# Optimization experiments

Measured on AMD Instinct MI355X. Metric: run time of the kernel, lower is better.

The kernel has to match this reference:

```python
import jax, jax.numpy as jnp
import numpy as np

NUM_GRAPHS = 2048
NODES_PER_GRAPH = 256
N_NODES = NUM_GRAPHS * NODES_PER_GRAPH
N_EDGES = 2 * N_NODES
F_IN = 768
HID = 128
N_CLS = 2


def setup_inputs() -> dict:
    key = jax.random.key(0)
    ks = jax.random.split(key, 12)
    x = jax.random.normal(ks[0], (N_NODES, F_IN), dtype=jnp.float32)
    edge_index = jax.random.randint(ks[1], (2, N_EDGES), 0, N_NODES, dtype=jnp.int32)
    batch = jnp.repeat(jnp.arange(NUM_GRAPHS, dtype=jnp.int32), NODES_PER_GRAPH)
    s = 1.0 / np.sqrt(F_IN)
    sh = 1.0 / np.sqrt(HID)
    s2h = 1.0 / np.sqrt(2 * HID)
    return {
        "x": x,
        "edge_index": edge_index,
        "batch": batch,
        # SAGEConv: lin_l (aggregated neighbors, with bias) + lin_r (root, no bias)
        "W_l": jax.random.uniform(ks[2], (F_IN, HID), jnp.float32, -s, s),
        "b_l": jax.random.uniform(ks[3], (HID,), jnp.float32, -s, s),
        "W_r": jax.random.uniform(ks[4], (F_IN, HID), jnp.float32, -s, s),
        "W0": jax.random.uniform(ks[5], (F_IN, HID), jnp.float32, -s, s),
        "b0": jax.random.uniform(ks[6], (HID,), jnp.float32, -s, s),
        "W1": jax.random.uniform(ks[7], (2 * HID, HID), jnp.float32, -s2h, s2h),
        "b1": jax.random.uniform(ks[8], (HID,), jnp.float32, -s2h, s2h),
        "W2": jax.random.uniform(ks[9], (HID, N_CLS), jnp.float32, -sh, sh),
        "b2": jax.random.uniform(ks[10], (HID,), jnp.float32, -sh, sh)[:N_CLS],
    }


def reference(x, edge_index, batch, W_l, b_l, W_r, W0, b0, W1, b1, W2, b2):
    n = x.shape[0]
    src, dst = edge_index[0], edge_index[1]
    # SAGEConv with mean aggregation: gather -> segment mean -> transform
    msg_sum = jax.ops.segment_sum(x[src], dst, num_segments=n)      # [N, F]
    cnt = jax.ops.segment_sum(jnp.ones((src.shape[0],), x.dtype), dst, num_segments=n)
    agg = msg_sum / jnp.maximum(cnt, 1.0)[:, None]
    h = jax.nn.relu(agg @ W_l + b_l + x @ W_r)                       # [N, H]
    # global max pool per graph
    pooled = jax.ops.segment_max(h, batch, num_segments=NUM_GRAPHS)  # [G, H]
    # root (news) node = first node of each graph (batch is sorted)
    roots = jnp.searchsorted(batch, jnp.arange(NUM_GRAPHS, dtype=batch.dtype))
    news = jax.nn.relu(x[roots] @ W0 + b0)                           # [G, H]
    z = jax.nn.relu(jnp.concatenate([pooled, news], axis=1) @ W1 + b1)
    return jax.nn.log_softmax(z @ W2 + b2, axis=-1)                  # [G, 2]
```

## Files before the change

### kernel.cpp

```cpp
#include <hip/hip_runtime.h>

#define NGRAPH 2048
#define NPG 256
#define NNODE (NGRAPH*NPG)
#define NEDGE (2*NNODE)
#define FIN 768
#define HID 128
#define SLOTS 64
#define BK 64
#define NKT (FIN/BK)

typedef __bf16 bf16x8 __attribute__((ext_vector_type(8)));
typedef __bf16 bf16x4 __attribute__((ext_vector_type(4)));
typedef float f32x4 __attribute__((ext_vector_type(4)));

__device__ __forceinline__ float bflo(unsigned v) {
    return __uint_as_float((v & 0xffffu) << 16);
}
__device__ __forceinline__ float bfhi(unsigned v) {
    return __uint_as_float(v & 0xffff0000u);
}

__global__ __launch_bounds__(256) void k_prep(
    const float* __restrict__ Wl, const float* __restrict__ Wr,
    const float* __restrict__ W0, __bf16* __restrict__ WbT,
    int* __restrict__ deg)
{
    int idx = blockIdx.x * 256 + threadIdx.x;
    deg[idx] = 0;
    if (idx < 384 * FIN) {
        int n = idx / FIN;
        int k = idx - n * FIN;
        float v;
        if (n < HID)            v = Wl[k * HID + n];
        else if (n < 2 * HID)   v = Wr[k * HID + (n - HID)];
        else                    v = W0[k * HID + (n - 2 * HID)];
        WbT[idx] = (__bf16)v;
    }
}

__global__ __launch_bounds__(512, 1) void k_gemm(
    const float* __restrict__ X, const __bf16* __restrict__ WbT,
    __bf16* __restrict__ Yl, __bf16* __restrict__ Yr,
    const int* __restrict__ ei, int* __restrict__ deg, int* __restrict__ elist)
{
    extern __shared__ __align__(16) char sm[];
    const int t = threadIdx.x;

    {
        int e = blockIdx.x * 512 + t;
        int src = ei[e];
        int dst = ei[NEDGE + e];
        int pos = atomicAdd(deg + dst, 1);
        if (pos < SLOTS) elist[(size_t)pos * NNODE + dst] = src;
    }

    const int lane = t & 63;
    const int w = t >> 6;
    const int wr = w >> 2;
    const int wc = w & 3;
    const size_t node0 = (size_t)blockIdx.x * 256;

    f32x4 acc[8][4];
#pragma unroll
    for (int m = 0; m < 8; ++m)
#pragma unroll
        for (int n = 0; n < 4; ++n)
            acc[m][n] = (f32x4){0.f, 0.f, 0.f, 0.f};

    const int arow = t >> 1;
    const int half = t & 1;
    const float* asrc = X + (node0 + arow) * FIN + half * 32;
    const int aswz = (arow & 7) << 4;
    int awoff[4];
#pragma unroll
    for (int j2 = 0; j2 < 4; ++j2)
        awoff[j2] = arow * 128 + (((half * 4 + j2) * 16) ^ aswz);

#define STAGE_B(kt, buf)                                                     \
    {                                                                        \
        _Pragma("unroll")                                                    \
        for (int r = 0; r < 4; ++r) {                                        \
            int idx = r * 512 + t;                                           \
            int bn = idx >> 3, bj = idx & 7;                                 \
            int koff = (bj ^ (bn & 7)) << 3;                                 \
            const __bf16* gp = WbT + bn * FIN + (kt) * BK + koff;            \
            __builtin_amdgcn_global_load_lds(                                \
                (__attribute__((address_space(1))) void*)gp,                 \
                (__attribute__((address_space(3))) void*)((buf) + 32768 + idx * 16),\
                16, 0, 0);                                                   \
        }                                                                    \
    }

    f32x4 q[8];
    STAGE_B(0, sm);
    {
        const f32x4* s4 = (const f32x4*)asrc;
#pragma unroll
        for (int i = 0; i < 8; ++i) q[i] = s4[i];
#pragma unroll
        for (int j2 = 0; j2 < 4; ++j2) {
            bf16x8 h;
#pragma unroll
            for (int i = 0; i < 4; ++i) {
                h[i]     = (__bf16)q[2 * j2][i];
                h[4 + i] = (__bf16)q[2 * j2 + 1][i];
            }
            *(bf16x8*)(sm + awoff[j2]) = h;
        }
    }
    __syncthreads();

    int cur = 0;
    for (int kt = 0; kt < NKT; ++kt) {
        char* bufC = sm + cur * 65536;
        char* bufN = sm + (cur ^ 1) * 65536;
        const bool more = (kt + 1 < NKT);

        if (more) {
            STAGE_B(kt + 1, bufN);
            __builtin_amdgcn_sched_barrier(0);
            const f32x4* s4 = (const f32x4*)(asrc + (kt + 1) * BK);
#pragma unroll
            for (int i = 0; i < 8; ++i) q[i] = s4[i];
            __builtin_amdgcn_sched_barrier(0);
        }

#pragma unroll
        for (int ks = 0; ks < 2; ++ks) {
            const int kb = ks * 64 + ((lane >> 4) << 4);
            bf16x8 a[8], b[4];
#pragma unroll
            for (int m = 0; m < 8; ++m) {
                int row = wr * 128 + m * 16 + (lane & 15);
                a[m] = *(const bf16x8*)(bufC + row * 128 + (kb ^ ((row & 7) << 4)));
            }
#pragma unroll
            for (int n = 0; n < 4; ++n) {
                int col = wc * 64 + n * 16 + (lane & 15);
                b[n] = *(const bf16x8*)(bufC + 32768 + col * 128 + (kb ^ ((col & 7) << 4)));
            }
#pragma unroll
            for (int m = 0; m < 8; ++m)
#pragma unroll
                for (int n = 0; n < 4; ++n)
                    acc[m][n] = __builtin_amdgcn_mfma_f32_16x16x32_bf16(
                        a[m], b[n], acc[m][n], 0, 0, 0);
        }

        if (more) {
#pragma unroll
            for (int j2 = 0; j2 < 4; ++j2) {
                bf16x8 h;
#pragma unroll
                for (int i = 0; i < 4; ++i) {
                    h[i]     = (__bf16)q[2 * j2][i];
                    h[4 + i] = (__bf16)q[2 * j2 + 1][i];
                }
                *(bf16x8*)(bufN + awoff[j2]) = h;
            }
        }
        __syncthreads();
        cur ^= 1;
    }

#pragma unroll
    for (int m = 0; m < 8; ++m) {
        const int rbase = wr * 128 + m * 16 + ((lane >> 4) << 2);
#pragma unroll
        for (int n = 0; n < 4; ++n) {
            const int col = wc * 64 + n * 16 + (lane & 15);
            __bf16* dst = (col < HID) ? Yl : Yr;
            const int c = col & (HID - 1);
#pragma unroll
            for (int j = 0; j < 4; ++j)
                dst[(node0 + rbase + j) * HID + c] = (__bf16)acc[m][n][j];
        }
    }
#undef STAGE_B
}

__global__ __launch_bounds__(512) void k_news(
    const float* __restrict__ X, const __bf16* __restrict__ W0bT,
    const float* __restrict__ b0, float* __restrict__ news)
{
    __shared__ __align__(16) char sm[12288];
    const int t = threadIdx.x;
    const int lane = t & 63;
    const int w = t >> 6;
    const int wr = w >> 2;
    const int wc = w & 3;
    const int g0 = blockIdx.x * 64;

    f32x4 acc[2][2];
#pragma unroll
    for (int m = 0; m < 2; ++m)
#pragma unroll
        for (int n = 0; n < 2; ++n)
            acc[m][n] = (f32x4){0.f, 0.f, 0.f, 0.f};

    const int arow = t >> 3;
    const int ak = (t & 7) * 4;
    const float* asrc = X + (size_t)(g0 + arow) * (NPG * FIN) + ak;
    const int aoff = arow * 64 + (((ak * 2) ^ (((arow >> 1) & 3) << 4)));

    for (int kt = 0; kt < FIN / 32; ++kt) {
        const int k0 = kt * 32;
        __syncthreads();
        {
            f32x4 p = *(const f32x4*)(asrc + k0);
            bf16x4 h;
#pragma unroll
            for (int i = 0; i < 4; ++i) h[i] = (__bf16)p[i];
            *(bf16x4*)(sm + aoff) = h;
        }
        {
            int bn = t >> 2;
            int bj = t & 3;
            int koff = (bj ^ ((bn >> 1) & 3)) << 3;
            const __bf16* g = W0bT + bn * FIN + k0 + koff;
            __builtin_amdgcn_global_load_lds(
                (__attribute__((address_space(1))) void*)g,
                (__attribute__((address_space(3))) void*)(sm + 4096 + t * 16),
                16, 0, 0);
        }
        __syncthreads();

        const int kb = (lane >> 4) << 4;
        bf16x8 a[2], b[2];
#pragma unroll
        for (int m = 0; m < 2; ++m) {
            int row = wr * 32 + m * 16 + (lane & 15);
            a[m] = *(const bf16x8*)(sm + row * 64 + (kb ^ (((row >> 1) & 3) << 4)));
        }
#pragma unroll
        for (int n = 0; n < 2; ++n) {
            int row = wc * 32 + n * 16 + (lane & 15);
            b[n] = *(const bf16x8*)(sm + 4096 + row * 64 + (kb ^ (((row >> 1) & 3) << 4)));
        }
#pragma unroll
        for (int m = 0; m < 2; ++m)
#pragma unroll
            for (int n = 0; n < 2; ++n)
                acc[m][n] = __builtin_amdgcn_mfma_f32_16x16x32_bf16(
                    a[m], b[n], acc[m][n], 0, 0, 0);
    }

#pragma unroll
    for (int m = 0; m < 2; ++m) {
        const int rbase = wr * 32 + m * 16 + ((lane >> 4) << 2);
#pragma unroll
        for (int n = 0; n < 2; ++n) {
            const int col = wc * 32 + n * 16 + (lane & 15);
            const float bb = b0[col];
#pragma unroll
            for (int j = 0; j < 4; ++j)
                news[(size_t)(g0 + rbase + j) * HID + col] =
                    fmaxf(acc[m][n][j] + bb, 0.f);
        }
    }
}

__global__ __launch_bounds__(512) void k_fused(
    const int* __restrict__ deg, const int* __restrict__ elist,
    const __bf16* __restrict__ Yl, const __bf16* __restrict__ Yr,
    const float* __restrict__ bl, const float* __restrict__ news,
    const float* __restrict__ W1, const float* __restrict__ b1,
    const float* __restrict__ W2, const float* __restrict__ b2,
    float* __restrict__ out)
{
    __shared__ int   sdeg[NPG];
    __shared__ int   sel[4 * NPG];
    __shared__ float red[8 * HID];
    __shared__ float cat[2 * HID];
    __shared__ float zs[HID];

    const int g = blockIdx.x;
    const int t = threadIdx.x;
    const size_t gbase = (size_t)g * NPG;

    if (t < NPG) sdeg[t] = deg[gbase + t];
#pragma unroll
    for (int r = 0; r < 2; ++r) {
        int idx = r * 512 + t;
        sel[idx] = elist[(size_t)(idx >> 8) * NNODE + gbase + (idx & 255)];
    }
    __syncthreads();

    const int l = t & 63;
    const int sub = t >> 6;
    const int half = l >> 5;
    const int lj = l & 31;
    const int d4 = lj * 4;
    const float4 blv = *(const float4*)(bl + d4);
    const uint2* yl2 = (const uint2*)Yl;
    const uint2* yr2 = (const uint2*)Yr;

    float m0 = -3.0e38f, m1 = -3.0e38f, m2 = -3.0e38f, m3 = -3.0e38f;

    for (int k4 = 0; k4 < 8; ++k4) {
        const int nA = sub + 8 * (4 * k4 + half);
        const int nB = sub + 8 * (4 * k4 + 2 + half);
        const int dgA = sdeg[nA], dgB = sdeg[nB];
        int sA[4], sB[4];
#pragma unroll
        for (int j = 0; j < 4; ++j) {
            int cA = sel[j * NPG + nA];
            int cB = sel[j * NPG + nB];
            sA[j] = (j < dgA) ? cA : 0;
            sB[j] = (j < dgB) ? cB : 0;
        }
        uint2 vA[4], vB[4];
#pragma unroll
        for (int j = 0; j < 4; ++j) {
            vA[j] = yl2[(size_t)sA[j] * 32 + lj];
            vB[j] = yl2[(size_t)sB[j] * 32 + lj];
        }
        const uint2 yA = yr2[(gbase + nA) * 32 + lj];
        const uint2 yB = yr2[(gbase + nB) * 32 + lj];

        float s0A = 0.f, s1A = 0.f, s2A = 0.f, s3A = 0.f;
        float s0B = 0.f, s1B = 0.f, s2B = 0.f, s3B = 0.f;
#pragma unroll
        for (int j = 0; j < 4; ++j) {
            const float mA = (j < dgA) ? 1.f : 0.f;
            const float mB = (j < dgB) ? 1.f : 0.f;
            s0A = fmaf(mA, bflo(vA[j].x), s0A);
            s1A = fmaf(mA, bfhi(vA[j].x), s1A);
            s2A = fmaf(mA, bflo(vA[j].y), s2A);
            s3A = fmaf(mA, bfhi(vA[j].y), s3A);
            s0B = fmaf(mB, bflo(vB[j].x), s0B);
            s1B = fmaf(mB, bfhi(vB[j].x), s1B);
            s2B = fmaf(mB, bflo(vB[j].y), s2B);
            s3B = fmaf(mB, bfhi(vB[j].y), s3B);
        }
        int mx = dgA > dgB ? dgA : dgB;
        mx = max(mx, __shfl_xor(mx, 32));
        mx = mx < SLOTS ? mx : SLOTS;
        for (int j = 4; j < mx; ++j) {
            int cA = elist[(size_t)j * NNODE + gbase + nA];
            int cB = elist[(size_t)j * NNODE + gbase + nB];
            int eA = (j < dgA) ? cA : 0;
            int eB = (j < dgB) ? cB : 0;
            uint2 wA = yl2[(size_t)eA * 32 + lj];
            uint2 wB = yl2[(size_t)eB * 32 + lj];
            const float mA = (j < dgA) ? 1.f : 0.f;
            const float mB = (j < dgB) ? 1.f : 0.f;
            s0A = fmaf(mA, bflo(wA.x), s0A);
            s1A = fmaf(mA, bfhi(wA.x), s1A);
            s2A = fmaf(mA, bflo(wA.y), s2A);
            s3A = fmaf(mA, bfhi(wA.y), s3A);
            s0B = fmaf(mB, bflo(wB.x), s0B);
            s1B = fmaf(mB, bfhi(wB.x), s1B);
            s2B = fmaf(mB, bflo(wB.y), s2B);
            s3B = fmaf(mB, bfhi(wB.y), s3B);
        }
        const float invA = 1.f / fmaxf((float)dgA, 1.f);
        const float invB = 1.f / fmaxf((float)dgB, 1.f);
        float h0 = fmaf(s0A, invA, blv.x) + bflo(yA.x);
        float h1 = fmaf(s1A, invA, blv.y) + bfhi(yA.x);
        float h2 = fmaf(s2A, invA, blv.z) + bflo(yA.y);
        float h3 = fmaf(s3A, invA, blv.w) + bfhi(yA.y);
        m0 = fmaxf(m0, fmaxf(h0, 0.f));
        m1 = fmaxf(m1, fmaxf(h1, 0.f));
        m2 = fmaxf(m2, fmaxf(h2, 0.f));
        m3 = fmaxf(m3, fmaxf(h3, 0.f));
        h0 = fmaf(s0B, invB, blv.x) + bflo(yB.x);
        h1 = fmaf(s1B, invB, blv.y) + bfhi(yB.x);
        h2 = fmaf(s2B, invB, blv.z) + bflo(yB.y);
        h3 = fmaf(s3B, invB, blv.w) + bfhi(yB.y);
        m0 = fmaxf(m0, fmaxf(h0, 0.f));
        m1 = fmaxf(m1, fmaxf(h1, 0.f));
        m2 = fmaxf(m2, fmaxf(h2, 0.f));
        m3 = fmaxf(m3, fmaxf(h3, 0.f));
    }
    m0 = fmaxf(m0, __shfl_xor(m0, 32));
    m1 = fmaxf(m1, __shfl_xor(m1, 32));
    m2 = fmaxf(m2, __shfl_xor(m2, 32));
    m3 = fmaxf(m3, __shfl_xor(m3, 32));
    if (half == 0) {
        float4 mv = {m0, m1, m2, m3};
        *(float4*)(red + sub * HID + d4) = mv;
    }
    __syncthreads();

    if (t < HID) {
        float v = red[t];
#pragma unroll
        for (int s = 1; s < 8; ++s) v = fmaxf(v, red[s * HID + t]);
        cat[t] = v;
        cat[HID + t] = news[(size_t)g * HID + t];
    }
    __syncthreads();

    if (t < HID) {
        float a0 = 0.f, a1 = 0.f, a2 = 0.f, a3 = 0.f;
        for (int k = 0; k < 2 * HID; k += 4) {
            a0 = fmaf(cat[k + 0], W1[(k + 0) * HID + t], a0);
            a1 = fmaf(cat[k + 1], W1[(k + 1) * HID + t], a1);
            a2 = fmaf(cat[k + 2], W1[(k + 2) * HID + t], a2);
            a3 = fmaf(cat[k + 3], W1[(k + 3) * HID + t], a3);
        }
        zs[t] = fmaxf((a0 + a1) + (a2 + a3) + b1[t], 0.f);
    }
    __syncthreads();

    if (t < 64) {
        float z0 = zs[t * 2], z1 = zs[t * 2 + 1];
        float p0 = fmaf(z0, W2[t * 4 + 0], z1 * W2[t * 4 + 2]);
        float p1 = fmaf(z0, W2[t * 4 + 1], z1 * W2[t * 4 + 3]);
#pragma unroll
        for (int off = 32; off; off >>= 1) {
            p0 += __shfl_down(p0, off);
            p1 += __shfl_down(p1, off);
        }
        if (t == 0) {
            float l0 = p0 + b2[0], l1 = p1 + b2[1];
            float mx = fmaxf(l0, l1);
            float lse = mx + logf(expf(l0 - mx) + expf(l1 - mx));
            out[(size_t)g * 2 + 0] = l0 - lse;
            out[(size_t)g * 2 + 1] = l1 - lse;
        }
    }
}

extern "C" void kernel_launch(void* const* d_in, const int* in_sizes, int n_in,
                              void* d_out, int out_size, void* d_ws, size_t ws_size,
                              hipStream_t stream)
{
    const float* x   = (const float*)d_in[0];
    const int*   ei  = (const int*)d_in[1];
    const float* W_l = (const float*)d_in[3];
    const float* b_l = (const float*)d_in[4];
    const float* W_r = (const float*)d_in[5];
    const float* W0  = (const float*)d_in[6];
    const float* b0  = (const float*)d_in[7];
    const float* W1  = (const float*)d_in[8];
    const float* b1  = (const float*)d_in[9];
    const float* W2  = (const float*)d_in[10];
    const float* b2  = (const float*)d_in[11];
    float* out = (float*)d_out;

    char* ws = (char*)d_ws;
    size_t off = 0;
    auto alloc = [&](size_t bytes) {
        char* p = ws + off;
        off += (bytes + 511) & ~(size_t)511;
        return p;
    };
    __bf16* WbT   = (__bf16*)alloc((size_t)384 * FIN * 2);
    __bf16* Yl    = (__bf16*)alloc((size_t)NNODE * HID * 2);
    __bf16* Yr    = (__bf16*)alloc((size_t)NNODE * HID * 2);
    int*    deg   = (int*)alloc((size_t)NNODE * 4);
    int*    elist = (int*)alloc((size_t)NNODE * SLOTS * 4);
    float*  news  = (float*)alloc((size_t)NGRAPH * HID * 4);
    if (off > ws_size) return;

    k_prep<<<NNODE / 256, 256, 0, stream>>>(W_l, W_r, W0, WbT, deg);
    k_gemm<<<NNODE / 256, 512, 131072, stream>>>(x, WbT, Yl, Yr, ei, deg, elist);
    k_news<<<NGRAPH / 64, 512, 0, stream>>>(x, WbT + (size_t)256 * FIN, b0, news);
    k_fused<<<NGRAPH, 512, 0, stream>>>(deg, elist, Yl, Yr, b_l, news,
                                        W1, b1, W2, b2, out);
}
```

Measured before the change: 668.8 us.

## Stage fp32 X tiles via direct-to-LDS loads and merge news GEMM into main kernel

The main GEMM now copies fp32 X tiles straight into LDS with global_load_lds, using a swizzled layout. The fp32-to-bf16 conversion moves to after the LDS read, and the weight operand is read directly from global memory into registers instead of being staged in LDS. This is meant to take the conversion and register round-trip off the critical path and let the load overlap the MFMA work. The small news GEMM becomes extra blocks of the same launch, removing one kernel launch. The cost is double the LDS traffic for the A operand, since it is now held as fp32, plus uncached global B reads in every tile step.

```diff
diff --git a/kernel.cpp b/kernel.cpp
--- a/kernel.cpp
+++ b/kernel.cpp
@@ -39,13 +39,149 @@
     }
 }
 
+#define AS1 __attribute__((address_space(1)))
+#define AS3 __attribute__((address_space(3)))
+
+template<bool MORE>
+__device__ __forceinline__ void tileF(
+    const char* rbuf, char* sbuf, int t, int lane, int wr, int wc,
+    const float* X, size_t node0, const __bf16* WbT, int kt,
+    f32x4 (&acc)[8][4])
+{
+    bf16x8 b[2][4];
+#pragma unroll
+    for (int ks = 0; ks < 2; ++ks)
+#pragma unroll
+        for (int n = 0; n < 4; ++n) {
+            int col = wc * 64 + n * 16 + (lane & 15);
+            b[ks][n] = *(const bf16x8*)(WbT + (size_t)col * FIN
+                                        + kt * BK + ks * 32 + ((lane >> 4) << 3));
+        }
+    __builtin_amdgcn_sched_barrier(0);
+    if constexpr (MORE) {
+#pragma unroll
+        for (int r = 0; r < 8; ++r) {
+            int idx = r * 512 + t;
+            int row = idx >> 4, s = idx & 15;
+            int koffb = (s * 16) ^ ((row & 7) << 5);
+            const float* g = X + (node0 + row) * FIN + (kt + 1) * BK + (koffb >> 2);
+            __builtin_amdgcn_global_load_lds(
+                (AS1 void*)g, (AS3 void*)(sbuf + idx * 16), 16, 0, 0);
+        }
+        __builtin_amdgcn_sched_barrier(0);
+    }
+#pragma unroll
+    for (int ks = 0; ks < 2; ++ks) {
+        bf16x8 a[8];
+#pragma unroll
+        for (int m = 0; m < 8; ++m) {
+            int row = wr * 128 + m * 16 + (lane & 15);
+            int off = row * 256 + ((ks * 128 + ((lane >> 4) << 5)) ^ ((row & 7) << 5));
+            f32x4 f0 = *(const f32x4*)(rbuf + off);
+            f32x4 f1 = *(const f32x4*)(rbuf + off + 16);
+#pragma unroll
+            for (int i = 0; i < 4; ++i) {
+                a[m][i]     = (__bf16)f0[i];
+                a[m][4 + i] = (__bf16)f1[i];
+            }
+        }
+#pragma unroll
+        for (int m = 0; m < 8; ++m)
+#pragma unroll
+            for (int n = 0; n < 4; ++n)
+                acc[m][n] = __builtin_amdgcn_mfma_f32_16x16x32_bf16(
+                    a[m], b[ks][n], acc[m][n], 0, 0, 0);
+    }
+    if constexpr (MORE) {
+        asm volatile("s_waitcnt vmcnt(0)" ::: "memory");
+        __builtin_amdgcn_s_barrier();
+    }
+}
+
 __global__ __launch_bounds__(512, 1) void k_gemm(
     const float* __restrict__ X, const __bf16* __restrict__ WbT,
     __bf16* __restrict__ Yl, __bf16* __restrict__ Yr,
-    const int* __restrict__ ei, int* __restrict__ deg, int* __restrict__ elist)
+    const int* __restrict__ ei, int* __restrict__ deg, int* __restrict__ elist,
+    const float* __restrict__ b0, float* __restrict__ news)
 {
     extern __shared__ __align__(16) char sm[];
     const int t = threadIdx.x;
+    const int lane = t & 63;
+    const int w = t >> 6;
+
+    if (blockIdx.x >= NNODE / 256) {
+        const int wr = w >> 2;
+        const int wc = w & 3;
+        const int g0 = (blockIdx.x - NNODE / 256) * 64;
+
+        f32x4 acc[2][2];
+#pragma unroll
+        for (int m = 0; m < 2; ++m)
+#pragma unroll
+            for (int n = 0; n < 2; ++n)
+                acc[m][n] = (f32x4){0.f, 0.f, 0.f, 0.f};
+
+        const int arow = t >> 3;
+        const int ak = (t & 7) * 4;
+        const float* asrc = X + (size_t)(g0 + arow) * (NPG * FIN) + ak;
+        const int aoff = arow * 64 + (((ak * 2) ^ (((arow >> 1) & 3) << 4)));
+        const __bf16* W0bT = WbT + (size_t)256 * FIN;
+
+        for (int kt = 0; kt < FIN / 32; ++kt) {
+            const int k0 = kt * 32;
+            __syncthreads();
+            {
+                f32x4 p = *(const f32x4*)(asrc + k0);
+                bf16x4 h;
+#pragma unroll
+                for (int i = 0; i < 4; ++i) h[i] = (__bf16)p[i];
+                *(bf16x4*)(sm + aoff) = h;
+            }
+            {
+                int bn = t >> 2;
+                int bj = t & 3;
+                int koff = (bj ^ ((bn >> 1) & 3)) << 3;
+                const __bf16* g = W0bT + bn * FIN + k0 + koff;
+                __builtin_amdgcn_global_load_lds(
+                    (AS1 void*)g, (AS3 void*)(sm + 4096 + t * 16), 16, 0, 0);
+            }
+            __syncthreads();
+
+            const int kb = (lane >> 4) << 4;
+            bf16x8 a[2], b[2];
+#pragma unroll
+            for (int m = 0; m < 2; ++m) {
+                int row = wr * 32 + m * 16 + (lane & 15);
+                a[m] = *(const bf16x8*)(sm + row * 64 + (kb ^ (((row >> 1) & 3) << 4)));
+            }
+#pragma unroll
+            for (int n = 0; n < 2; ++n) {
+                int row = wc * 32 + n * 16 + (lane & 15);
+                b[n] = *(const bf16x8*)(sm + 4096 + row * 64 + (kb ^ (((row >> 1) & 3) << 4)));
+            }
+#pragma unroll
+            for (int m = 0; m < 2; ++m)
+#pragma unroll
+                for (int n = 0; n < 2; ++n)
+                    acc[m][n] = __builtin_amdgcn_mfma_f32_16x16x32_bf16(
+                        a[m], b[n], acc[m][n], 0, 0, 0);
+        }
+
+#pragma unroll
+        for (int m = 0; m < 2; ++m) {
+            const int rbase = wr * 32 + m * 16 + ((lane >> 4) << 2);
+#pragma unroll
+            for (int n = 0; n < 2; ++n) {
+                const int col = wc * 32 + n * 16 + (lane & 15);
+                const float bb = b0[col];
+#pragma unroll
+                for (int j = 0; j < 4; ++j)
+                    news[(size_t)(g0 + rbase + j) * HID + col] =
+                        fmaxf(acc[m][n][j] + bb, 0.f);
+            }
+        }
+        return;
+    }
 
     {
         int e = blockIdx.x * 512 + t;
@@ -55,8 +191,6 @@
         if (pos < SLOTS) elist[(size_t)pos * NNODE + dst] = src;
     }
 
-    const int lane = t & 63;
-    const int w = t >> 6;
     const int wr = w >> 2;
     const int wc = w & 3;
     const size_t node0 = (size_t)blockIdx.x * 256;
@@ -68,101 +202,35 @@
         for (int n = 0; n < 4; ++n)
             acc[m][n] = (f32x4){0.f, 0.f, 0.f, 0.f};
 
-    const int arow = t >> 1;
-    const int half = t & 1;
-    const float* asrc = X + (node0 + arow) * FIN + half * 32;
-    const int aswz = (arow & 7) << 4;
-    int awoff[4];
-#pragma unroll
-    for (int j2 = 0; j2 < 4; ++j2)
-        awoff[j2] = arow * 128 + (((half * 4 + j2) * 16) ^ aswz);
-
-#define STAGE_B(kt, buf)                                                     \
-    {                                                                        \
-        _Pragma("unroll")                                                    \
-        for (int r = 0; r < 4; ++r) {                                        \
-            int idx = r * 512 + t;                                           \
-            int bn = idx >> 3, bj = idx & 7;                                 \
-            int koff = (bj ^ (bn & 7)) << 3;                                 \
-            const __bf16* gp = WbT + bn * FIN + (kt) * BK + koff;            \
-            __builtin_amdgcn_global_load_lds(                                \
-                (__attribute__((address_space(1))) void*)gp,                 \
-                (__attribute__((address_space(3))) void*)((buf) + 32768 + idx * 16),\
-                16, 0, 0);                                                   \
-        }                                                                    \
-    }
-
-    f32x4 q[8];
-    STAGE_B(0, sm);
+    char* buf0 = sm;
+    char* buf1 = sm + 65536;
+
     {
-        const f32x4* s4 = (const f32x4*)asrc;
-#pragma unroll
-        for (int i = 0; i < 8; ++i) q[i] = s4[i];
-#pragma unroll
-        for (int j2 = 0; j2 < 4; ++j2) {
-            bf16x8 h;
-#pragma unroll
-            for (int i = 0; i < 4; ++i) {
-                h[i]     = (__bf16)q[2 * j2][i];
-                h[4 + i] = (__bf16)q[2 * j2 + 1][i];
-            }
-            *(bf16x8*)(sm + awoff[j2]) = h;
-        }
-    }
-    __syncthreads();
-
-    int cur = 0;
-    for (int kt = 0; kt < NKT; ++kt) {
-        char* bufC = sm + cur * 65536;
-        char* bufN = sm + (cur ^ 1) * 65536;
-        const bool more = (kt + 1 < NKT);
-
-        if (more) {
-            STAGE_B(kt + 1, bufN);
-            __builtin_amdgcn_sched_barrier(0);
-            const f32x4* s4 = (const f32x4*)(asrc + (kt + 1) * BK);
-#pragma unroll
-            for (int i = 0; i < 8; ++i) q[i] = s4[i];
-            __builtin_amdgcn_sched_barrier(0);
-        }
-
-#pragma unroll
-        for (int ks = 0; ks < 2; ++ks) {
-            const int kb = ks * 64 + ((lane >> 4) << 4);
-            bf16x8 a[8], b[4];
-#pragma unroll
-            for (int m = 0; m < 8; ++m) {
-                int row = wr * 128 + m * 16 + (lane & 15);
-                a[m] = *(const bf16x8*)(bufC + row * 128 + (kb ^ ((row & 7) << 4)));
-            }
-#pragma unroll
-            for (int n = 0; n < 4; ++n) {
-                int col = wc * 64 + n * 16 + (lane & 15);
-                b[n] = *(const bf16x8*)(bufC + 32768 + col * 128 + (kb ^ ((col & 7) << 4)));
-            }
-#pragma unroll
-            for (int m = 0; m < 8; ++m)
-#pragma unroll
-                for (int n = 0; n < 4; ++n)
-                    acc[m][n] = __builtin_amdgcn_mfma_f32_16x16x32_bf16(
-                        a[m], b[n], acc[m][n], 0, 0, 0);
-        }
-
-        if (more) {
-#pragma unroll
-            for (int j2 = 0; j2 < 4; ++j2) {
-                bf16x8 h;
-#pragma unroll
-                for (int i = 0; i < 4; ++i) {
-                    h[i]     = (__bf16)q[2 * j2][i];
-                    h[4 + i] = (__bf16)q[2 * j2 + 1][i];
-                }
-                *(bf16x8*)(bufN + awoff[j2]) = h;
-            }
-        }
-        __syncthreads();
-        cur ^= 1;
-    }
+#pragma unroll
+        for (int r = 0; r < 8; ++r) {
+            int idx = r * 512 + t;
+            int row = idx >> 4, s = idx & 15;
+            int koffb = (s * 16) ^ ((row & 7) << 5);
+            const float* g = X + (node0 + row) * FIN + 0 * BK + (koffb >> 2);
+            __builtin_amdgcn_global_load_lds(
+                (AS1 void*)g, (AS3 void*)(buf0 + idx * 16), 16, 0, 0);
+        }
+        asm volatile("s_waitcnt vmcnt(0)" ::: "memory");
+        __builtin_amdgcn_s_barrier();
+    }
+
+    tileF<true >(buf0, buf1, t, lane, wr, wc, X, node0, WbT, 0,  acc);
+    tileF<true >(buf1, buf0, t, lane, wr, wc, X, node0, WbT, 1,  acc);
+    tileF<true >(buf0, buf1, t, lane, wr, wc, X, node0, WbT, 2,  acc);
+    tileF<true >(buf1, buf0, t, lane, wr, wc, X, node0, WbT, 3,  acc);
+    tileF<true >(buf0, buf1, t, lane, wr, wc, X, node0, WbT, 4,  acc);
+    tileF<true >(buf1, buf0, t, lane, wr, wc, X, node0, WbT, 5,  acc);
+    tileF<true >(buf0, buf1, t, lane, wr, wc, X, node0, WbT, 6,  acc);
+    tileF<true >(buf1, buf0, t, lane, wr, wc, X, node0, WbT, 7,  acc);
+    tileF<true >(buf0, buf1, t, lane, wr, wc, X, node0, WbT, 8,  acc);
+    tileF<true >(buf1, buf0, t, lane, wr, wc, X, node0, WbT, 9,  acc);
+    tileF<true >(buf0, buf1, t, lane, wr, wc, X, node0, WbT, 10, acc);
+    tileF<false>(buf1, buf0, t, lane, wr, wc, X, node0, WbT, 11, acc);
 
 #pragma unroll
     for (int m = 0; m < 8; ++m) {
@@ -175,88 +243,6 @@
 #pragma unroll
             for (int j = 0; j < 4; ++j)
                 dst[(node0 + rbase + j) * HID + c] = (__bf16)acc[m][n][j];
-        }
-    }
-#undef STAGE_B
-}
-
-__global__ __launch_bounds__(512) void k_news(
-    const float* __restrict__ X, const __bf16* __restrict__ W0bT,
-    const float* __restrict__ b0, float* __restrict__ news)
-{
-    __shared__ __align__(16) char sm[12288];
-    const int t = threadIdx.x;
-    const int lane = t & 63;
-    const int w = t >> 6;
-    const int wr = w >> 2;
-    const int wc = w & 3;
-    const int g0 = blockIdx.x * 64;
-
-    f32x4 acc[2][2];
-#pragma unroll
-    for (int m = 0; m < 2; ++m)
-#pragma unroll
-        for (int n = 0; n < 2; ++n)
-            acc[m][n] = (f32x4){0.f, 0.f, 0.f, 0.f};
-
-    const int arow = t >> 3;
-    const int ak = (t & 7) * 4;
-    const float* asrc = X + (size_t)(g0 + arow) * (NPG * FIN) + ak;
-    const int aoff = arow * 64 + (((ak * 2) ^ (((arow >> 1) & 3) << 4)));
-
-    for (int kt = 0; kt < FIN / 32; ++kt) {
-        const int k0 = kt * 32;
-        __syncthreads();
-        {
-            f32x4 p = *(const f32x4*)(asrc + k0);
-            bf16x4 h;
-#pragma unroll
-            for (int i = 0; i < 4; ++i) h[i] = (__bf16)p[i];
-            *(bf16x4*)(sm + aoff) = h;
-        }
-        {
-            int bn = t >> 2;
-            int bj = t & 3;
-            int koff = (bj ^ ((bn >> 1) & 3)) << 3;
-            const __bf16* g = W0bT + bn * FIN + k0 + koff;
-            __builtin_amdgcn_global_load_lds(
-                (__attribute__((address_space(1))) void*)g,
-                (__attribute__((address_space(3))) void*)(sm + 4096 + t * 16),
-                16, 0, 0);
-        }
-        __syncthreads();
-
-        const int kb = (lane >> 4) << 4;
-        bf16x8 a[2], b[2];
-#pragma unroll
-        for (int m = 0; m < 2; ++m) {
-            int row = wr * 32 + m * 16 + (lane & 15);
-            a[m] = *(const bf16x8*)(sm + row * 64 + (kb ^ (((row >> 1) & 3) << 4)));
-        }
-#pragma unroll
-        for (int n = 0; n < 2; ++n) {
-            int row = wc * 32 + n * 16 + (lane & 15);
-            b[n] = *(const bf16x8*)(sm + 4096 + row * 64 + (kb ^ (((row >> 1) & 3) << 4)));
-        }
-#pragma unroll
-        for (int m = 0; m < 2; ++m)
-#pragma unroll
-            for (int n = 0; n < 2; ++n)
-                acc[m][n] = __builtin_amdgcn_mfma_f32_16x16x32_bf16(
-                    a[m], b[n], acc[m][n], 0, 0, 0);
-    }
-
-#pragma unroll
-    for (int m = 0; m < 2; ++m) {
-        const int rbase = wr * 32 + m * 16 + ((lane >> 4) << 2);
-#pragma unroll
-        for (int n = 0; n < 2; ++n) {
-            const int col = wc * 32 + n * 16 + (lane & 15);
-            const float bb = b0[col];
-#pragma unroll
-            for (int j = 0; j < 4; ++j)
-                news[(size_t)(g0 + rbase + j) * HID + col] =
-                    fmaxf(acc[m][n][j] + bb, 0.f);
         }
     }
 }
@@ -457,8 +443,8 @@
     if (off > ws_size) return;
 
     k_prep<<<NNODE / 256, 256, 0, stream>>>(W_l, W_r, W0, WbT, deg);
-    k_gemm<<<NNODE / 256, 512, 131072, stream>>>(x, WbT, Yl, Yr, ei, deg, elist);
-    k_news<<<NGRAPH / 64, 512, 0, stream>>>(x, WbT + (size_t)256 * FIN, b0, news);
+    k_gemm<<<NNODE / 256 + NGRAPH / 64, 512, 131072, stream>>>(
+        x, WbT, Yl, Yr, ei, deg, elist, b0, news);
     k_fused<<<NGRAPH, 512, 0, stream>>>(deg, elist, Yl, Yr, b_l, news,
                                         W1, b1, W2, b2, out);
 }
```

Result: faster. 634.4 us (-5.1%).
